# Optimization experiments

Hardware: AMD Instinct MI355X
Metric: run time of the kernel (lower is better)

## Reference

```python
import jax, jax.numpy as jnp
import numpy as np

B, S, H = 1, 1024, 1024
E = 1024          # expert_dim
NEXP = 16         # num_experts
TOPK = 2
ALPHA = 1.702
LIMIT = 7.0


def setup_inputs() -> dict:
    key = jax.random.key(0)
    ks = jax.random.split(key, 8)
    hidden_states = jax.random.normal(ks[0], (B, S, H), dtype=jnp.float32)
    # router (gate): Linear(H, NEXP) with bias
    Wg = jax.random.normal(ks[1], (NEXP, H), dtype=jnp.float32) / np.sqrt(H)
    bg = jax.random.normal(ks[2], (NEXP,), dtype=jnp.float32) * 0.01
    # per-expert gate_up_proj: Linear(H, 2E) -> store as [NEXP, H, 2E]
    Wgu = jax.random.normal(ks[3], (NEXP, H, 2 * E), dtype=jnp.float32) / np.sqrt(H)
    bgu = jax.random.normal(ks[4], (NEXP, 2 * E), dtype=jnp.float32) * 0.01
    # per-expert down_proj: Linear(E, H) -> store as [NEXP, E, H]
    Wd = jax.random.normal(ks[5], (NEXP, E, H), dtype=jnp.float32) / np.sqrt(E)
    bd = jax.random.normal(ks[6], (NEXP, H), dtype=jnp.float32) * 0.01
    return {"hidden_states": hidden_states, "Wg": Wg, "bg": bg,
            "Wgu": Wgu, "bgu": bgu, "Wd": Wd, "bd": bd}


def _moe_forward(x, Wg, bg, Wgu, bgu, Wd, bd):
    b, s, h = x.shape
    xt = x.reshape(-1, h)                                   # [T, H]
    # router
    logits = xt @ Wg.T + bg                                 # [T, NEXP]
    # gpt_oss routing: topk over raw logits, softmax over selected
    top_vals, top_idx = jax.lax.top_k(logits, TOPK)         # [T, K]
    rw = jax.nn.softmax(top_vals.astype(jnp.float32), axis=-1).astype(xt.dtype)
    # combine weight per (token, expert): zero for unselected experts
    onehot = jax.nn.one_hot(top_idx, NEXP, dtype=xt.dtype)  # [T, K, NEXP]
    cw = jnp.einsum("tk,tke->te", rw, onehot)               # [T, NEXP]
    # dense expert compute (reference math identical to gather/scatter version)
    gu = jnp.einsum("th,ehf->tef", xt, Wgu) + bgu[None]     # [T, NEXP, 2E]
    gate = gu[..., ::2]
    up = gu[..., 1::2]
    gate = jnp.minimum(gate, LIMIT)
    up = jnp.clip(up, -LIMIT, LIMIT)
    glu = gate * jax.nn.sigmoid(gate * ALPHA)
    gated = (up + 1.0) * glu                                # [T, NEXP, E]
    out_e = jnp.einsum("tef,efh->teh", gated, Wd) + bd[None]  # [T, NEXP, H]
    out = jnp.einsum("teh,te->th", out_e, cw)               # [T, H]
    return out.reshape(b, s, h)


def reference(hidden_states, Wg, bg, Wgu, bgu, Wd, bd):
    return _moe_forward(hidden_states, Wg, bg, Wgu, bgu, Wd, bd)
```

## Files before the change

kernel.cpp:

```cpp
#include <hip/hip_runtime.h>
#include <hip/hip_bf16.h>

#define NT 1024
#define HD 1024
#define ED 1024
#define F2D 2048
#define NEXPERT 16
#define GROWS 2304
#define ALPHA_C 1.702f
#define LIMIT_C 7.0f

typedef float f32x4 __attribute__((ext_vector_type(4)));
typedef short short8 __attribute__((ext_vector_type(8)));
typedef unsigned int u32x4 __attribute__((ext_vector_type(4)));

__device__ __forceinline__ unsigned short f2bf(float x) {
  union { float f; unsigned int u; } v; v.f = x;
  unsigned int r = v.u + 0x7FFFu + ((v.u >> 16) & 1u);
  return (unsigned short)(r >> 16);
}
__device__ __forceinline__ unsigned int pk2(float lo, float hi) {
  return (unsigned int)f2bf(lo) | ((unsigned int)f2bf(hi) << 16);
}
__device__ __forceinline__ void async16(const void* g, void* l) {
  __builtin_amdgcn_global_load_lds((const __attribute__((address_space(1))) void*)g,
                                   (__attribute__((address_space(3))) void*)l, 16, 0, 0);
}

__global__ __launch_bounds__(64) void k_router(const float* __restrict__ x,
                                               const float* __restrict__ Wg,
                                               const float* __restrict__ bg,
                                               const float* __restrict__ bd,
                                               int* __restrict__ e01,
                                               float* __restrict__ w0f,
                                               float* __restrict__ w1f,
                                               unsigned short* __restrict__ Xbf,
                                               float* __restrict__ out) {
  const int t = blockIdx.x;
  const int l = threadIdx.x;
  const float4* x4 = (const float4*)(x + (size_t)t * HD);
  for (int i = 0; i < 4; ++i) {
    const int idx = l + 64 * i;
    float4 v = x4[idx];
    unsigned int a = pk2(v.x, v.y);
    unsigned int b = pk2(v.z, v.w);
    unsigned int* dst = (unsigned int*)(Xbf + (size_t)t * HD + idx * 4);
    dst[0] = a; dst[1] = b;
  }
  const int e = l & 15, qq = l >> 4;
  const float4* wg4 = (const float4*)(Wg + (size_t)e * HD);
  float s = 0.f;
  for (int j = 0; j < 64; ++j) {
    const int idx = qq + 4 * j;
    float4 a = x4[idx], b = wg4[idx];
    s += a.x * b.x + a.y * b.y + a.z * b.z + a.w * b.w;
  }
  s += __shfl_xor(s, 16);
  s += __shfl_xor(s, 32);
  const float logit = s + bg[e];
  float v0 = -1e30f, v1 = -1e30f; int i0 = 0, i1 = 0;
  for (int k = 0; k < 16; ++k) {
    float lv = __shfl(logit, k);
    if (lv > v0) { v1 = v0; i1 = i0; v0 = lv; i0 = k; }
    else if (lv > v1) { v1 = lv; i1 = k; }
  }
  const float w0 = 1.f / (1.f + __expf(v1 - v0));
  const float w1 = 1.f - w0;
  if (l == 0) {
    e01[t] = i0 | (i1 << 8);
    w0f[t] = w0;
    w1f[t] = w1;
  }
  const float4* bd0 = (const float4*)(bd + (size_t)i0 * HD);
  const float4* bd1 = (const float4*)(bd + (size_t)i1 * HD);
  float4* o4 = (float4*)(out + (size_t)t * HD);
  for (int i = 0; i < 4; ++i) {
    const int idx = l + 64 * i;
    float4 a = bd0[idx], b = bd1[idx];
    float4 r;
    r.x = w0 * a.x + w1 * b.x;
    r.y = w0 * a.y + w1 * b.y;
    r.z = w0 * a.z + w1 * b.z;
    r.w = w0 * a.w + w1 * b.w;
    o4[idx] = r;
  }
}

__global__ __launch_bounds__(1024) void k_scan(const int* __restrict__ e01,
                                               const float* __restrict__ w0f,
                                               const float* __restrict__ w1f,
                                               int* __restrict__ cnt,
                                               int* __restrict__ off,
                                               int* __restrict__ gtok,
                                               float* __restrict__ gwt) {
  __shared__ int scnt[NEXPERT];
  __shared__ int soff[NEXPERT];
  __shared__ int scur[NEXPERT];
  const int t = threadIdx.x;
  if (t < NEXPERT) { scnt[t] = 0; scur[t] = 0; }
  __syncthreads();
  const int p = e01[t];
  const int e0 = p & 255, e1 = p >> 8;
  atomicAdd(&scnt[e0], 1);
  atomicAdd(&scnt[e1], 1);
  __syncthreads();
  if (t == 0) {
    int a = 0;
    for (int e = 0; e < NEXPERT; ++e) { soff[e] = a; off[e] = a; cnt[e] = scnt[e]; a += scnt[e]; }
  }
  __syncthreads();
  int s0 = atomicAdd(&scur[e0], 1);
  gtok[soff[e0] + s0] = t; gwt[soff[e0] + s0] = w0f[t];
  int s1 = atomicAdd(&scur[e1], 1);
  gtok[soff[e1] + s1] = t; gwt[soff[e1] + s1] = w1f[t];
}

#define BST1 260
__global__ __launch_bounds__(256, 2) void k_gemm1(const unsigned short* __restrict__ Xbf,
                                                  const float* __restrict__ Wgu,
                                                  const float* __restrict__ bgu,
                                                  const int* __restrict__ cnt,
                                                  const int* __restrict__ off,
                                                  const int* __restrict__ gtok,
                                                  unsigned short* __restrict__ Gact) {
  const int e = blockIdx.z;
  const int Ne = cnt[e];
  const int mtile = blockIdx.y;
  if (mtile * 64 >= Ne) return;
  const int ntile = blockIdx.x;
  const int tid = threadIdx.x;
  const int lane = tid & 63;
  const int wv = tid >> 6;
  const int q = lane >> 4;
  const int fr = lane & 15;
  const int base = off[e] + mtile * 64;

  __shared__ unsigned short Alds[2][64 * 32];
  __shared__ unsigned int Blds[2][16 * BST1];

  const int arow = wv * 16 + (lane >> 2);
  const int ags = base + (((mtile * 64 + arow) < Ne) ? arow : 0);
  const unsigned short* agp = Xbf + (size_t)gtok[ags] * HD + (lane & 3) * 8;
  const int aofs = wv * 512;

  const float* Wb = Wgu + (size_t)e * HD * F2D + (size_t)(wv * 8) * F2D + ntile * 256 + lane * 4;

  f32x4 acc[4][4] = {};
  float4 br[8];

#pragma unroll
  for (int j = 0; j < 8; ++j) br[j] = *(const float4*)(Wb + (size_t)j * F2D);
  async16(agp, Alds[0] + aofs);
#pragma unroll
  for (int p = 0; p < 4; ++p) {
    u32x4 pkv;
    pkv[0] = pk2(br[2 * p].x, br[2 * p + 1].x);
    pkv[1] = pk2(br[2 * p].y, br[2 * p + 1].y);
    pkv[2] = pk2(br[2 * p].z, br[2 * p + 1].z);
    pkv[3] = pk2(br[2 * p].w, br[2 * p + 1].w);
    *(u32x4*)(Blds[0] + (wv * 4 + p) * BST1 + lane * 4) = pkv;
  }
  __syncthreads();

  for (int ks = 0; ks < 32; ++ks) {
    const int cur = ks & 1, nxt = cur ^ 1;
    const bool more = (ks + 1) < 32;
    if (more) {
      const float* bp = Wb + (size_t)(ks + 1) * 32 * F2D;
#pragma unroll
      for (int j = 0; j < 8; ++j) br[j] = *(const float4*)(bp + (size_t)j * F2D);
      async16(agp + (ks + 1) * 32, Alds[nxt] + aofs);
    }
    short8 af[4], bfr[4];
#pragma unroll
    for (int mi = 0; mi < 4; ++mi)
      af[mi] = *(const short8*)(Alds[cur] + (mi * 16 + fr) * 32 + q * 8);
#pragma unroll
    for (int ni = 0; ni < 4; ++ni) {
      const unsigned int* p = Blds[cur] + q * 4 * BST1 + wv * 64 + ni * 16 + fr;
      union { unsigned int u[4]; short8 s; } uu;
      uu.u[0] = p[0]; uu.u[1] = p[BST1]; uu.u[2] = p[2 * BST1]; uu.u[3] = p[3 * BST1];
      bfr[ni] = uu.s;
    }
#pragma unroll
    for (int mi = 0; mi < 4; ++mi)
#pragma unroll
      for (int ni = 0; ni < 4; ++ni)
        acc[mi][ni] = __builtin_amdgcn_mfma_f32_16x16x32_bf16(af[mi], bfr[ni], acc[mi][ni], 0, 0, 0);
    if (more) {
#pragma unroll
      for (int p = 0; p < 4; ++p) {
        u32x4 pkv;
        pkv[0] = pk2(br[2 * p].x, br[2 * p + 1].x);
        pkv[1] = pk2(br[2 * p].y, br[2 * p + 1].y);
        pkv[2] = pk2(br[2 * p].z, br[2 * p + 1].z);
        pkv[3] = pk2(br[2 * p].w, br[2 * p + 1].w);
        *(u32x4*)(Blds[nxt] + (wv * 4 + p) * BST1 + lane * 4) = pkv;
      }
    }
    __syncthreads();
  }

  const float* bguE = bgu + (size_t)e * F2D + ntile * 256;
#pragma unroll
  for (int mi = 0; mi < 4; ++mi) {
#pragma unroll
    for (int ni = 0; ni < 4; ++ni) {
      const int col = wv * 64 + ni * 16 + fr;
      const float bias = bguE[col];
#pragma unroll
      for (int r = 0; r < 4; ++r) {
        const int srow = mi * 16 + q * 4 + r;
        float v = acc[mi][ni][r] + bias;
        float pv = __shfl_xor(v, 1);
        float gate = (lane & 1) ? pv : v;
        float up   = (lane & 1) ? v : pv;
        gate = fminf(gate, LIMIT_C);
        up = fminf(fmaxf(up, -LIMIT_C), LIMIT_C);
        float glu = gate / (1.f + __expf(-ALPHA_C * gate));
        float val = (up + 1.f) * glu;
        if (!(lane & 1) && (mtile * 64 + srow) < Ne)
          Gact[(size_t)(base + srow) * ED + ((ntile * 256 + col) >> 1)] = f2bf(val);
      }
    }
  }
}

#define BST2 132
__global__ __launch_bounds__(256, 2) void k_gemm2(const unsigned short* __restrict__ Gact,
                                                  const float* __restrict__ Wd,
                                                  const int* __restrict__ cnt,
                                                  const int* __restrict__ off,
                                                  const int* __restrict__ gtok,
                                                  const float* __restrict__ gwt,
                                                  float* __restrict__ out) {
  const int e = blockIdx.z;
  const int Ne = cnt[e];
  const int mtile = blockIdx.y;
  if (mtile * 64 >= Ne) return;
  const int ntile = blockIdx.x;
  const int tid = threadIdx.x;
  const int lane = tid & 63;
  const int wv = tid >> 6;
  const int q = lane >> 4;
  const int fr = lane & 15;
  const int base = off[e] + mtile * 64;

  __shared__ unsigned short Alds[2][64 * 32];
  __shared__ unsigned int Blds[2][16 * BST2];

  const int arow = wv * 16 + (lane >> 2);
  const unsigned short* agp = Gact + (size_t)(base + arow) * ED + (lane & 3) * 8;
  const int aofs = wv * 512;

  const int brow0 = wv * 8 + (lane >> 5) * 4;
  const int bcol = (lane & 31) * 4;
  const float* Wb = Wd + (size_t)e * ED * HD + (size_t)brow0 * HD + ntile * 128 + bcol;

  f32x4 acc[4][2] = {};
  float4 br[4];

#pragma unroll
  for (int j = 0; j < 4; ++j) br[j] = *(const float4*)(Wb + (size_t)j * HD);
  async16(agp, Alds[0] + aofs);
#pragma unroll
  for (int p = 0; p < 2; ++p) {
    u32x4 pkv;
    pkv[0] = pk2(br[2 * p].x, br[2 * p + 1].x);
    pkv[1] = pk2(br[2 * p].y, br[2 * p + 1].y);
    pkv[2] = pk2(br[2 * p].z, br[2 * p + 1].z);
    pkv[3] = pk2(br[2 * p].w, br[2 * p + 1].w);
    *(u32x4*)(Blds[0] + (brow0 / 2 + p) * BST2 + bcol) = pkv;
  }
  __syncthreads();

  for (int ks = 0; ks < 32; ++ks) {
    const int cur = ks & 1, nxt = cur ^ 1;
    const bool more = (ks + 1) < 32;
    if (more) {
      const float* bp = Wb + (size_t)(ks + 1) * 32 * HD;
#pragma unroll
      for (int j = 0; j < 4; ++j) br[j] = *(const float4*)(bp + (size_t)j * HD);
      async16(agp + (ks + 1) * 32, Alds[nxt] + aofs);
    }
    short8 af[4], bfr[2];
#pragma unroll
    for (int mi = 0; mi < 4; ++mi)
      af[mi] = *(const short8*)(Alds[cur] + (mi * 16 + fr) * 32 + q * 8);
#pragma unroll
    for (int ni = 0; ni < 2; ++ni) {
      const unsigned int* p = Blds[cur] + q * 4 * BST2 + wv * 32 + ni * 16 + fr;
      union { unsigned int u[4]; short8 s; } uu;
      uu.u[0] = p[0]; uu.u[1] = p[BST2]; uu.u[2] = p[2 * BST2]; uu.u[3] = p[3 * BST2];
      bfr[ni] = uu.s;
    }
#pragma unroll
    for (int mi = 0; mi < 4; ++mi)
#pragma unroll
      for (int ni = 0; ni < 2; ++ni)
        acc[mi][ni] = __builtin_amdgcn_mfma_f32_16x16x32_bf16(af[mi], bfr[ni], acc[mi][ni], 0, 0, 0);
    if (more) {
#pragma unroll
      for (int p = 0; p < 2; ++p) {
        u32x4 pkv;
        pkv[0] = pk2(br[2 * p].x, br[2 * p + 1].x);
        pkv[1] = pk2(br[2 * p].y, br[2 * p + 1].y);
        pkv[2] = pk2(br[2 * p].z, br[2 * p + 1].z);
        pkv[3] = pk2(br[2 * p].w, br[2 * p + 1].w);
        *(u32x4*)(Blds[nxt] + (brow0 / 2 + p) * BST2 + bcol) = pkv;
      }
    }
    __syncthreads();
  }

#pragma unroll
  for (int mi = 0; mi < 4; ++mi) {
#pragma unroll
    for (int r = 0; r < 4; ++r) {
      const int srow = mi * 16 + q * 4 + r;
      if ((mtile * 64 + srow) < Ne) {
        const int gsl = base + srow;
        const int tok = gtok[gsl];
        const float wt = gwt[gsl];
        float* op = out + (size_t)tok * HD + ntile * 128;
#pragma unroll
        for (int ni = 0; ni < 2; ++ni) {
          const int col = wv * 32 + ni * 16 + fr;
          atomicAdd(op + col, wt * acc[mi][ni][r]);
        }
      }
    }
  }
}

extern "C" void kernel_launch(void* const* d_in, const int* in_sizes, int n_in,
                              void* d_out, int out_size, void* d_ws, size_t ws_size,
                              hipStream_t stream) {
  const float* x   = (const float*)d_in[0];
  const float* Wg  = (const float*)d_in[1];
  const float* bg  = (const float*)d_in[2];
  const float* Wgu = (const float*)d_in[3];
  const float* bgu = (const float*)d_in[4];
  const float* Wd  = (const float*)d_in[5];
  const float* bd  = (const float*)d_in[6];
  float* out = (float*)d_out;

  int* cnt = (int*)d_ws;
  int* off = cnt + 16;
  int* e01 = off + 16;
  float* w0f = (float*)(e01 + NT);
  float* w1f = w0f + NT;
  int* gtok = (int*)(w1f + NT);
  float* gwt = (float*)(gtok + GROWS);
  unsigned short* Xbf = (unsigned short*)(gwt + GROWS);
  unsigned short* Gact = Xbf + (size_t)NT * HD;

  k_router<<<NT, 64, 0, stream>>>(x, Wg, bg, bd, e01, w0f, w1f, Xbf, out);
  k_scan<<<1, NT, 0, stream>>>(e01, w0f, w1f, cnt, off, gtok, gwt);
  k_gemm1<<<dim3(8, 16, NEXPERT), 256, 0, stream>>>(Xbf, Wgu, bgu, cnt, off, gtok, Gact);
  k_gemm2<<<dim3(8, 16, NEXPERT), 256, 0, stream>>>(Gact, Wd, cnt, off, gtok, gwt, out);
}
```

Measured before the change: 379.2 us.

## Enlarge expert GEMM M-tiles so each weight tile is streamed once

Both expert GEMMs grow the per-block token tile from 64 to 256 rows. The N tiles are retuned (gemm1 uses 128 columns with 8 waves in a 4x2 layout, gemm2 uses 64 columns with 4 waves), and the grid shrinks to two M tiles per expert. The goal is to load and bf16-convert each fp32 expert weight tile once per expert instead of once per 64-token slice, which cuts redundant weight traffic. Weight loads also become nontemporal so the streamed weights do not pollute the cache. In exchange there are far fewer active blocks, and experts that receive more than 512 tokens would no longer be fully covered.

```diff
diff --git a/kernel.cpp b/kernel.cpp
--- a/kernel.cpp
+++ b/kernel.cpp
@@ -11,6 +11,7 @@
 #define LIMIT_C 7.0f
 
 typedef float f32x4 __attribute__((ext_vector_type(4)));
+typedef float fv4 __attribute__((ext_vector_type(4)));
 typedef short short8 __attribute__((ext_vector_type(8)));
 typedef unsigned int u32x4 __attribute__((ext_vector_type(4)));
 
@@ -21,6 +22,9 @@
 }
 __device__ __forceinline__ unsigned int pk2(float lo, float hi) {
   return (unsigned int)f2bf(lo) | ((unsigned int)f2bf(hi) << 16);
+}
+__device__ __forceinline__ fv4 ldnt4(const float* p) {
+  return __builtin_nontemporal_load((const fv4*)p);
 }
 __device__ __forceinline__ void async16(const void* g, void* l) {
   __builtin_amdgcn_global_load_lds((const __attribute__((address_space(1))) void*)g,
@@ -115,8 +119,8 @@
   gtok[soff[e1] + s1] = t; gwt[soff[e1] + s1] = w1f[t];
 }
 
-#define BST1 260
-__global__ __launch_bounds__(256, 2) void k_gemm1(const unsigned short* __restrict__ Xbf,
+#define BSTG1 132
+__global__ __launch_bounds__(512, 2) void k_gemm1(const unsigned short* __restrict__ Xbf,
                                                   const float* __restrict__ Wgu,
                                                   const float* __restrict__ bgu,
                                                   const int* __restrict__ cnt,
@@ -126,39 +130,44 @@
   const int e = blockIdx.z;
   const int Ne = cnt[e];
   const int mtile = blockIdx.y;
-  if (mtile * 64 >= Ne) return;
+  if (mtile * 256 >= Ne) return;
   const int ntile = blockIdx.x;
   const int tid = threadIdx.x;
   const int lane = tid & 63;
   const int wv = tid >> 6;
+  const int wm = wv >> 1;
+  const int wn = wv & 1;
   const int q = lane >> 4;
   const int fr = lane & 15;
-  const int base = off[e] + mtile * 64;
-
-  __shared__ unsigned short Alds[2][64 * 32];
-  __shared__ unsigned int Blds[2][16 * BST1];
-
-  const int arow = wv * 16 + (lane >> 2);
-  const int ags = base + (((mtile * 64 + arow) < Ne) ? arow : 0);
-  const unsigned short* agp = Xbf + (size_t)gtok[ags] * HD + (lane & 3) * 8;
-  const int aofs = wv * 512;
-
-  const float* Wb = Wgu + (size_t)e * HD * F2D + (size_t)(wv * 8) * F2D + ntile * 256 + lane * 4;
+  const int base = off[e] + mtile * 256;
+
+  __shared__ unsigned short Alds[2][256 * 32];
+  __shared__ unsigned int Blds[2][16 * BSTG1];
+
+  const int ar0 = wv * 32 + (lane >> 2);
+  const int ar1 = ar0 + 16;
+  const int ags0 = base + (((mtile * 256 + ar0) < Ne) ? ar0 : 0);
+  const int ags1 = base + (((mtile * 256 + ar1) < Ne) ? ar1 : 0);
+  const unsigned short* agp0 = Xbf + (size_t)gtok[ags0] * HD + (lane & 3) * 8;
+  const unsigned short* agp1 = Xbf + (size_t)gtok[ags1] * HD + (lane & 3) * 8;
+  const int aofs = wv * 1024;
+
+  const int p2 = tid >> 5;
+  const int bc = tid & 31;
+  const float* Wb = Wgu + (size_t)e * HD * F2D + (size_t)(2 * p2) * F2D + ntile * 128 + bc * 4;
 
   f32x4 acc[4][4] = {};
-  float4 br[8];
-
-#pragma unroll
-  for (int j = 0; j < 8; ++j) br[j] = *(const float4*)(Wb + (size_t)j * F2D);
-  async16(agp, Alds[0] + aofs);
-#pragma unroll
-  for (int p = 0; p < 4; ++p) {
+  fv4 b0, b1;
+
+  b0 = ldnt4(Wb);
+  b1 = ldnt4(Wb + F2D);
+  async16(agp0, Alds[0] + aofs);
+  async16(agp1, Alds[0] + aofs + 512);
+  {
     u32x4 pkv;
-    pkv[0] = pk2(br[2 * p].x, br[2 * p + 1].x);
-    pkv[1] = pk2(br[2 * p].y, br[2 * p + 1].y);
-    pkv[2] = pk2(br[2 * p].z, br[2 * p + 1].z);
-    pkv[3] = pk2(br[2 * p].w, br[2 * p + 1].w);
-    *(u32x4*)(Blds[0] + (wv * 4 + p) * BST1 + lane * 4) = pkv;
+    pkv[0] = pk2(b0[0], b1[0]); pkv[1] = pk2(b0[1], b1[1]);
+    pkv[2] = pk2(b0[2], b1[2]); pkv[3] = pk2(b0[3], b1[3]);
+    *(u32x4*)(Blds[0] + p2 * BSTG1 + bc * 4) = pkv;
   }
   __syncthreads();
 
@@ -167,19 +176,20 @@
     const bool more = (ks + 1) < 32;
     if (more) {
       const float* bp = Wb + (size_t)(ks + 1) * 32 * F2D;
-#pragma unroll
-      for (int j = 0; j < 8; ++j) br[j] = *(const float4*)(bp + (size_t)j * F2D);
-      async16(agp + (ks + 1) * 32, Alds[nxt] + aofs);
+      b0 = ldnt4(bp);
+      b1 = ldnt4(bp + F2D);
+      async16(agp0 + (ks + 1) * 32, Alds[nxt] + aofs);
+      async16(agp1 + (ks + 1) * 32, Alds[nxt] + aofs + 512);
     }
     short8 af[4], bfr[4];
 #pragma unroll
     for (int mi = 0; mi < 4; ++mi)
-      af[mi] = *(const short8*)(Alds[cur] + (mi * 16 + fr) * 32 + q * 8);
+      af[mi] = *(const short8*)(Alds[cur] + (wm * 64 + mi * 16 + fr) * 32 + q * 8);
 #pragma unroll
     for (int ni = 0; ni < 4; ++ni) {
-      const unsigned int* p = Blds[cur] + q * 4 * BST1 + wv * 64 + ni * 16 + fr;
+      const unsigned int* p = Blds[cur] + (q * 4) * BSTG1 + wn * 64 + ni * 16 + fr;
       union { unsigned int u[4]; short8 s; } uu;
-      uu.u[0] = p[0]; uu.u[1] = p[BST1]; uu.u[2] = p[2 * BST1]; uu.u[3] = p[3 * BST1];
+      uu.u[0] = p[0]; uu.u[1] = p[BSTG1]; uu.u[2] = p[2 * BSTG1]; uu.u[3] = p[3 * BSTG1];
       bfr[ni] = uu.s;
     }
 #pragma unroll
@@ -188,29 +198,24 @@
       for (int ni = 0; ni < 4; ++ni)
         acc[mi][ni] = __builtin_amdgcn_mfma_f32_16x16x32_bf16(af[mi], bfr[ni], acc[mi][ni], 0, 0, 0);
     if (more) {
-#pragma unroll
-      for (int p = 0; p < 4; ++p) {
-        u32x4 pkv;
-        pkv[0] = pk2(br[2 * p].x, br[2 * p + 1].x);
-        pkv[1] = pk2(br[2 * p].y, br[2 * p + 1].y);
-        pkv[2] = pk2(br[2 * p].z, br[2 * p + 1].z);
-        pkv[3] = pk2(br[2 * p].w, br[2 * p + 1].w);
-        *(u32x4*)(Blds[nxt] + (wv * 4 + p) * BST1 + lane * 4) = pkv;
-      }
+      u32x4 pkv;
+      pkv[0] = pk2(b0[0], b1[0]); pkv[1] = pk2(b0[1], b1[1]);
+      pkv[2] = pk2(b0[2], b1[2]); pkv[3] = pk2(b0[3], b1[3]);
+      *(u32x4*)(Blds[nxt] + p2 * BSTG1 + bc * 4) = pkv;
     }
     __syncthreads();
   }
 
-  const float* bguE = bgu + (size_t)e * F2D + ntile * 256;
+  const float* bguE = bgu + (size_t)e * F2D + ntile * 128;
 #pragma unroll
   for (int mi = 0; mi < 4; ++mi) {
 #pragma unroll
     for (int ni = 0; ni < 4; ++ni) {
-      const int col = wv * 64 + ni * 16 + fr;
-      const float bias = bguE[col];
+      const int coll = wn * 64 + ni * 16 + fr;
+      const float bias = bguE[coll];
 #pragma unroll
       for (int r = 0; r < 4; ++r) {
-        const int srow = mi * 16 + q * 4 + r;
+        const int srow = wm * 64 + mi * 16 + q * 4 + r;
         float v = acc[mi][ni][r] + bias;
         float pv = __shfl_xor(v, 1);
         float gate = (lane & 1) ? pv : v;
@@ -219,14 +224,14 @@
         up = fminf(fmaxf(up, -LIMIT_C), LIMIT_C);
         float glu = gate / (1.f + __expf(-ALPHA_C * gate));
         float val = (up + 1.f) * glu;
-        if (!(lane & 1) && (mtile * 64 + srow) < Ne)
-          Gact[(size_t)(base + srow) * ED + ((ntile * 256 + col) >> 1)] = f2bf(val);
+        if (!(lane & 1) && (mtile * 256 + srow) < Ne)
+          Gact[(size_t)(base + srow) * ED + ((ntile * 128 + coll) >> 1)] = f2bf(val);
       }
     }
   }
 }
 
-#define BST2 132
+#define BSTG2 68
 __global__ __launch_bounds__(256, 2) void k_gemm2(const unsigned short* __restrict__ Gact,
                                                   const float* __restrict__ Wd,
                                                   const int* __restrict__ cnt,
@@ -237,40 +242,39 @@
   const int e = blockIdx.z;
   const int Ne = cnt[e];
   const int mtile = blockIdx.y;
-  if (mtile * 64 >= Ne) return;
+  if (mtile * 256 >= Ne) return;
   const int ntile = blockIdx.x;
   const int tid = threadIdx.x;
   const int lane = tid & 63;
   const int wv = tid >> 6;
   const int q = lane >> 4;
   const int fr = lane & 15;
-  const int base = off[e] + mtile * 64;
-
-  __shared__ unsigned short Alds[2][64 * 32];
-  __shared__ unsigned int Blds[2][16 * BST2];
-
-  const int arow = wv * 16 + (lane >> 2);
-  const unsigned short* agp = Gact + (size_t)(base + arow) * ED + (lane & 3) * 8;
-  const int aofs = wv * 512;
-
-  const int brow0 = wv * 8 + (lane >> 5) * 4;
-  const int bcol = (lane & 31) * 4;
-  const float* Wb = Wd + (size_t)e * ED * HD + (size_t)brow0 * HD + ntile * 128 + bcol;
-
-  f32x4 acc[4][2] = {};
-  float4 br[4];
-
-#pragma unroll
-  for (int j = 0; j < 4; ++j) br[j] = *(const float4*)(Wb + (size_t)j * HD);
-  async16(agp, Alds[0] + aofs);
-#pragma unroll
-  for (int p = 0; p < 2; ++p) {
+  const int base = off[e] + mtile * 256;
+
+  __shared__ unsigned short Alds[2][256 * 32];
+  __shared__ unsigned int Blds[2][16 * BSTG2];
+
+  const int arb = wv * 64 + (lane >> 2);
+  const unsigned short* agp = Gact + (size_t)(base + arb) * ED + (lane & 3) * 8;
+  const int aofs = wv * 2048;
+
+  const int p2 = tid >> 4;
+  const int bc = tid & 15;
+  const float* Wb = Wd + (size_t)e * ED * HD + (size_t)(2 * p2) * HD + ntile * 64 + bc * 4;
+
+  f32x4 acc[4][4] = {};
+  fv4 b0, b1;
+
+  b0 = ldnt4(Wb);
+  b1 = ldnt4(Wb + HD);
+#pragma unroll
+  for (int j = 0; j < 4; ++j)
+    async16(agp + (size_t)j * 16 * ED, Alds[0] + aofs + j * 512);
+  {
     u32x4 pkv;
-    pkv[0] = pk2(br[2 * p].x, br[2 * p + 1].x);
-    pkv[1] = pk2(br[2 * p].y, br[2 * p + 1].y);
-    pkv[2] = pk2(br[2 * p].z, br[2 * p + 1].z);
-    pkv[3] = pk2(br[2 * p].w, br[2 * p + 1].w);
-    *(u32x4*)(Blds[0] + (brow0 / 2 + p) * BST2 + bcol) = pkv;
+    pkv[0] = pk2(b0[0], b1[0]); pkv[1] = pk2(b0[1], b1[1]);
+    pkv[2] = pk2(b0[2], b1[2]); pkv[3] = pk2(b0[3], b1[3]);
+    *(u32x4*)(Blds[0] + p2 * BSTG2 + bc * 4) = pkv;
   }
   __syncthreads();
 
@@ -279,36 +283,33 @@
     const bool more = (ks + 1) < 32;
     if (more) {
       const float* bp = Wb + (size_t)(ks + 1) * 32 * HD;
-#pragma unroll
-      for (int j = 0; j < 4; ++j) br[j] = *(const float4*)(bp + (size_t)j * HD);
-      async16(agp + (ks + 1) * 32, Alds[nxt] + aofs);
-    }
-    short8 af[4], bfr[2];
+      b0 = ldnt4(bp);
+      b1 = ldnt4(bp + HD);
+#pragma unroll
+      for (int j = 0; j < 4; ++j)
+        async16(agp + (ks + 1) * 32 + (size_t)j * 16 * ED, Alds[nxt] + aofs + j * 512);
+    }
+    short8 af[4], bfr[4];
 #pragma unroll
     for (int mi = 0; mi < 4; ++mi)
-      af[mi] = *(const short8*)(Alds[cur] + (mi * 16 + fr) * 32 + q * 8);
-#pragma unroll
-    for (int ni = 0; ni < 2; ++ni) {
-      const unsigned int* p = Blds[cur] + q * 4 * BST2 + wv * 32 + ni * 16 + fr;
+      af[mi] = *(const short8*)(Alds[cur] + (wv * 64 + mi * 16 + fr) * 32 + q * 8);
+#pragma unroll
+    for (int ni = 0; ni < 4; ++ni) {
+      const unsigned int* p = Blds[cur] + (q * 4) * BSTG2 + ni * 16 + fr;
       union { unsigned int u[4]; short8 s; } uu;
-      uu.u[0] = p[0]; uu.u[1] = p[BST2]; uu.u[2] = p[2 * BST2]; uu.u[3] = p[3 * BST2];
+      uu.u[0] = p[0]; uu.u[1] = p[BSTG2]; uu.u[2] = p[2 * BSTG2]; uu.u[3] = p[3 * BSTG2];
       bfr[ni] = uu.s;
     }
 #pragma unroll
     for (int mi = 0; mi < 4; ++mi)
 #pragma unroll
-      for (int ni = 0; ni < 2; ++ni)
+      for (int ni = 0; ni < 4; ++ni)
         acc[mi][ni] = __builtin_amdgcn_mfma_f32_16x16x32_bf16(af[mi], bfr[ni], acc[mi][ni], 0, 0, 0);
     if (more) {
-#pragma unroll
-      for (int p = 0; p < 2; ++p) {
-        u32x4 pkv;
-        pkv[0] = pk2(br[2 * p].x, br[2 * p + 1].x);
-        pkv[1] = pk2(br[2 * p].y, br[2 * p + 1].y);
-        pkv[2] = pk2(br[2 * p].z, br[2 * p + 1].z);
-        pkv[3] = pk2(br[2 * p].w, br[2 * p + 1].w);
-        *(u32x4*)(Blds[nxt] + (brow0 / 2 + p) * BST2 + bcol) = pkv;
-      }
+      u32x4 pkv;
+      pkv[0] = pk2(b0[0], b1[0]); pkv[1] = pk2(b0[1], b1[1]);
+      pkv[2] = pk2(b0[2], b1[2]); pkv[3] = pk2(b0[3], b1[3]);
+      *(u32x4*)(Blds[nxt] + p2 * BSTG2 + bc * 4) = pkv;
     }
     __syncthreads();
   }
@@ -317,15 +318,15 @@
   for (int mi = 0; mi < 4; ++mi) {
 #pragma unroll
     for (int r = 0; r < 4; ++r) {
-      const int srow = mi * 16 + q * 4 + r;
-      if ((mtile * 64 + srow) < Ne) {
+      const int srow = wv * 64 + mi * 16 + q * 4 + r;
+      if ((mtile * 256 + srow) < Ne) {
         const int gsl = base + srow;
         const int tok = gtok[gsl];
         const float wt = gwt[gsl];
-        float* op = out + (size_t)tok * HD + ntile * 128;
-#pragma unroll
-        for (int ni = 0; ni < 2; ++ni) {
-          const int col = wv * 32 + ni * 16 + fr;
+        float* op = out + (size_t)tok * HD + ntile * 64;
+#pragma unroll
+        for (int ni = 0; ni < 4; ++ni) {
+          const int col = ni * 16 + fr;
           atomicAdd(op + col, wt * acc[mi][ni][r]);
         }
       }
@@ -357,6 +358,6 @@
 
   k_router<<<NT, 64, 0, stream>>>(x, Wg, bg, bd, e01, w0f, w1f, Xbf, out);
   k_scan<<<1, NT, 0, stream>>>(e01, w0f, w1f, cnt, off, gtok, gwt);
-  k_gemm1<<<dim3(8, 16, NEXPERT), 256, 0, stream>>>(Xbf, Wgu, bgu, cnt, off, gtok, Gact);
-  k_gemm2<<<dim3(8, 16, NEXPERT), 256, 0, stream>>>(Gact, Wd, cnt, off, gtok, gwt, out);
-}
+  k_gemm1<<<dim3(16, 2, NEXPERT), 512, 0, stream>>>(Xbf, Wgu, bgu, cnt, off, gtok, Gact);
+  k_gemm2<<<dim3(16, 2, NEXPERT), 256, 0, stream>>>(Gact, Wd, cnt, off, gtok, gwt, out);
+}
```

New measurement: 341.5 us. 1.11x faster.
